# Kernel optimization log

Hardware: AMD Instinct MI355X
Metric: run time of the kernel (lower is better)

## Reference

```python
import jax, jax.numpy as jnp
import numpy as np

D_MODEL = 2048
D_INNER = 4096
D_XB = 1024
D_STATE = 64
HEADDIM = 64
NHEADS = D_INNER // HEADDIM      # 64
NXB = D_XB // HEADDIM
D_CONV = 4
CHUNK = 128
EPS = 1e-5
D_FF = 8192
CONV_DIM = D_XB + D_XB + D_INNER             # conv over [x, B, C]
D_IN_PROJ = D_INNER + D_XB + D_XB + D_INNER + NHEADS  # z, x, B, C, dt


def setup_inputs() -> dict:
    key = jax.random.key(0)
    ks = jax.random.split(key, 8)
    s = 0.02
    return {
        "hidden_states": jax.random.normal(ks[0], (2, 2048, D_MODEL), jnp.float32),
        "in_proj_w": jax.random.normal(ks[1], (D_MODEL, D_IN_PROJ), jnp.float32) * s,
        "conv_w": jax.random.normal(ks[2], (CONV_DIM, D_CONV), jnp.float32) * 0.1,
        "conv_b": jnp.zeros((CONV_DIM,), jnp.float32),
        "dt_bias": jnp.log(jnp.expm1(jnp.linspace(0.001, 0.1, NHEADS, dtype=jnp.float32))),
        "A_log": jnp.log(jnp.linspace(1.0, 16.0, NHEADS, dtype=jnp.float32)),
        "D": jnp.ones((NHEADS,), jnp.float32),
        "norm_w": jnp.ones((D_INNER,), jnp.float32),
        "out_proj_w": jax.random.normal(ks[3], (D_INNER, D_MODEL), jnp.float32) * s,
        "ln1_w": jnp.ones((D_MODEL,), jnp.float32),
        "ln2_w": jnp.ones((D_MODEL,), jnp.float32),
        "gate_w": jax.random.normal(ks[4], (D_MODEL, D_FF), jnp.float32) * s,
        "up_w": jax.random.normal(ks[5], (D_MODEL, D_FF), jnp.float32) * s,
        "down_w": jax.random.normal(ks[6], (D_FF, D_MODEL), jnp.float32) * s,
    }


def rmsnorm(x, w, eps=EPS):
    return x * jax.lax.rsqrt(jnp.mean(x * x, axis=-1, keepdims=True) + eps) * w


def causal_depthwise_conv(x, w, b):
    # x: [b, l, c], w: [c, k] depthwise causal conv
    k = w.shape[1]
    xp = jnp.pad(x, ((0, 0), (k - 1, 0), (0, 0)))
    out = jax.lax.conv_general_dilated(
        xp.transpose(0, 2, 1), w[:, None, :], (1,), "VALID",
        feature_group_count=x.shape[-1])
    return out.transpose(0, 2, 1) + b


def ssd_chunked(xdt, dA, Bm, Cm):
    # Mamba2 SSD chunked scan. xdt: [b,l,h,p] (x*dt), dA: [b,l,h] (dt*A), Bm/Cm: [b,l,h,n]
    b, l, h, p = xdt.shape
    n = Bm.shape[-1]
    c, q = l // CHUNK, CHUNK
    xdt = xdt.reshape(b, c, q, h, p)
    Bm = Bm.reshape(b, c, q, h, n)
    Cm = Cm.reshape(b, c, q, h, n)
    dA = dA.reshape(b, c, q, h).transpose(0, 3, 1, 2)   # [b,h,c,q]
    dAc = jnp.cumsum(dA, axis=-1)                        # [b,h,c,q]
    # intra-chunk (diagonal blocks)
    seg = dAc[..., :, None] - dAc[..., None, :]          # [b,h,c,q,q]
    mask = jnp.tril(jnp.ones((q, q), bool))
    Lm = jnp.where(mask, jnp.exp(seg), 0.0)
    Y_diag = jnp.einsum("bcqhn,bcshn,bhcqs,bcshp->bcqhp", Cm, Bm, Lm, xdt)
    # per-chunk final states
    decay_states = jnp.exp(dAc[..., -1:] - dAc)          # [b,h,c,q]
    states = jnp.einsum("bcqhn,bhcq,bcqhp->bchpn", Bm, decay_states, xdt)
    chunk_decay = jnp.exp(dAc[..., -1])                  # [b,h,c]
    def step(carry, inp):
        s, d = inp
        new = s + d[:, :, None, None] * carry
        return new, carry
    init = jnp.zeros((b, h, p, n), xdt.dtype)
    _, prevs = jax.lax.scan(step, init,
                            (states.transpose(1, 0, 2, 3, 4),
                             chunk_decay.transpose(2, 0, 1)))
    # prevs: [c,b,h,p,n] = state entering each chunk; inter-chunk contribution
    Y_off = jnp.einsum("bcqhn,cbhpn,bhcq->bcqhp", Cm, prevs, jnp.exp(dAc))
    return (Y_diag + Y_off).reshape(b, l, h, p)


def mamba2(x, in_proj_w, conv_w, conv_b, dt_bias, A_log, Dp, norm_w, out_proj_w):
    b, l, _ = x.shape
    zxbcdt = x @ in_proj_w
    z, xb, Bc, Cc, dt = jnp.split(
        zxbcdt, [D_INNER, D_INNER + D_XB, D_INNER + 2 * D_XB, 2 * D_INNER + 2 * D_XB], axis=-1)
    xBC = jax.nn.silu(causal_depthwise_conv(jnp.concatenate([xb, Bc, Cc], -1), conv_w, conv_b))
    xb, Bc, Cc = jnp.split(xBC, [D_XB, 2 * D_XB], axis=-1)
    dt = jax.nn.softplus(dt + dt_bias)                   # [b,l,h]
    A = -jnp.exp(A_log)                                  # [h]
    rep = NHEADS // NXB
    x_h = jnp.repeat(xb.reshape(b, l, NXB, HEADDIM), rep, axis=2)   # [b,l,h,p]
    B_h = jnp.repeat(Bc.reshape(b, l, NXB, D_STATE), rep, axis=2)   # [b,l,h,n]
    C_h = Cc.reshape(b, l, NHEADS, D_STATE)
    y = ssd_chunked(x_h * dt[..., None], dt * A, B_h, C_h)
    y = y + Dp[None, None, :, None] * x_h
    y = y.reshape(b, l, D_INNER)
    y = rmsnorm(y * jax.nn.silu(z), norm_w)
    return y @ out_proj_w


def reference(hidden_states, in_proj_w, conv_w, conv_b, dt_bias, A_log, D,
              norm_w, out_proj_w, ln1_w, ln2_w, gate_w, up_w, down_w):
    residual = hidden_states
    h = rmsnorm(hidden_states, ln1_w)
    h = residual + mamba2(h, in_proj_w, conv_w, conv_b, dt_bias, A_log, D, norm_w, out_proj_w)
    residual = h
    h2 = rmsnorm(h, ln2_w)
    mlp = (jax.nn.silu(h2 @ gate_w) * (h2 @ up_w)) @ down_w
    return residual + mlp
```

## Files before the change

kernel.cpp:

```cpp
#include <hip/hip_runtime.h>
#include <hip/hip_bf16.h>
#include <stdint.h>

#define TOK     4096
#define LSEQ    2048
#define DMODEL  2048
#define DINNER  4096
#define DXB     1024
#define DIP     10304
#define NPROJ   10240
#define CONVDIM 6144
#define DFF     8192
#define NH      64
#define CHUNK   128
#define NCHUNK  16
#define EPSF    1e-5f

typedef __hip_bfloat16 bf16_t;
typedef __bf16 bf16x8 __attribute__((ext_vector_type(8)));
typedef float f32x4 __attribute__((ext_vector_type(4)));

__device__ __forceinline__ float siluf(float x) { return x / (1.f + __expf(-x)); }
__device__ __forceinline__ float bf2f(bf16_t h) { return __bfloat162float(h); }
__device__ __forceinline__ float bits2f(unsigned short u) { return __uint_as_float((unsigned)u << 16); }
__device__ __forceinline__ unsigned short f2bits(float f) {
  union { bf16_t h; unsigned short u; } cv; cv.h = __float2bfloat16(f); return cv.u;
}
__device__ __forceinline__ void gload_lds16(const void* g, void* l) {
  __builtin_amdgcn_global_load_lds((const __attribute__((address_space(1))) void*)g,
                                   (__attribute__((address_space(3))) void*)l, 16, 0, 0);
}

__global__ void k_tcvt(const float* __restrict__ in, bf16_t* __restrict__ out,
                       int R, int C, int rs, int r_off, int c_off) {
  __shared__ float tile[32][33];
  int c0 = blockIdx.x * 32, r0 = blockIdx.y * 32;
  int tx = threadIdx.x, ty = threadIdx.y;
  for (int i = 0; i < 32; i += 8)
    tile[ty + i][tx] = in[(size_t)(r_off + r0 + ty + i) * rs + c_off + c0 + tx];
  __syncthreads();
  for (int i = 0; i < 32; i += 8)
    out[(size_t)(c0 + ty + i) * R + r0 + tx] = __float2bfloat16(tile[tx][ty + i]);
}

__global__ __launch_bounds__(256) void k_rmsnorm_bf16(const float* __restrict__ x,
                                                      const float* __restrict__ w,
                                                      bf16_t* __restrict__ out, int D) {
  int row = blockIdx.x, tid = threadIdx.x;
  const float* xr = x + (size_t)row * D;
  float ss = 0.f;
  for (int j = tid; j < D; j += 256) { float v = xr[j]; ss += v * v; }
  __shared__ float sbuf[4];
  for (int o = 32; o > 0; o >>= 1) ss += __shfl_down(ss, o, 64);
  if ((tid & 63) == 0) sbuf[tid >> 6] = ss;
  __syncthreads();
  float rinv = rsqrtf((sbuf[0] + sbuf[1] + sbuf[2] + sbuf[3]) / D + EPSF);
  bf16_t* orow = out + (size_t)row * D;
  for (int j = tid; j < D; j += 256) orow[j] = __float2bfloat16(xr[j] * rinv * w[j]);
}

__global__ __launch_bounds__(256) void k_gemm(const bf16_t* __restrict__ A,
                                              const bf16_t* __restrict__ Bt,
                                              const float* auxf,
                                              void* outp, void* out2,
                                              int M, int N, int K, int mode) {
  __shared__ unsigned short As[128][32];
  __shared__ unsigned short Bs[128][32];
  const int tid = threadIdx.x;
  const int n0 = blockIdx.x * 128, m0 = blockIdx.y * 128;
  const int lane = tid & 63, w = tid >> 6;
  const int wm = (w >> 1) * 64, wn = (w & 1) * 64;
  const int l16 = lane & 15, quad = lane >> 4;

  const int srow = lane >> 2;
  const int scol = (lane & 3) * 8;
  const unsigned short* Ag = (const unsigned short*)A + (size_t)(m0 + w * 32 + srow) * K + scol;
  const unsigned short* Bg = (const unsigned short*)Bt + (size_t)(n0 + w * 32 + srow) * K + scol;
  const size_t K16 = (size_t)16 * K;
  unsigned short* lA0 = &As[w * 32][0];
  unsigned short* lA1 = &As[w * 32 + 16][0];
  unsigned short* lB0 = &Bs[w * 32][0];
  unsigned short* lB1 = &Bs[w * 32 + 16][0];

  f32x4 acc[4][4] = {};
  for (int k0 = 0; k0 < K; k0 += 32) {
    __syncthreads();
    gload_lds16(Ag, lA0); gload_lds16(Ag + K16, lA1);
    gload_lds16(Bg, lB0); gload_lds16(Bg + K16, lB1);
    Ag += 32; Bg += 32;
    __syncthreads();
    bf16x8 af[4], bfv[4];
#pragma unroll
    for (int mi = 0; mi < 4; mi++) af[mi] = *(const bf16x8*)&As[wm + mi * 16 + l16][quad * 8];
#pragma unroll
    for (int ni = 0; ni < 4; ni++) bfv[ni] = *(const bf16x8*)&Bs[wn + ni * 16 + l16][quad * 8];
#pragma unroll
    for (int mi = 0; mi < 4; mi++)
#pragma unroll
      for (int ni = 0; ni < 4; ni++)
        acc[mi][ni] = __builtin_amdgcn_mfma_f32_16x16x32_bf16(af[mi], bfv[ni], acc[mi][ni], 0, 0, 0);
  }
#pragma unroll
  for (int mi = 0; mi < 4; mi++) {
    const int gm = m0 + wm + mi * 16 + quad * 4;
#pragma unroll
    for (int ni = 0; ni < 4; ni++) {
      const int gn = n0 + wn + ni * 16 + l16;
#pragma unroll
      for (int r = 0; r < 4; r++) {
        const size_t idx = (size_t)(gm + r) * N + gn;
        float v = acc[mi][ni][r];
        if (mode == 0) {
          ((float*)outp)[idx] = v + (auxf ? auxf[idx] : 0.f);
        } else if (mode == 1) {
          ((bf16_t*)outp)[idx] = __float2bfloat16(siluf(v));
        } else if (mode == 2) {
          bf16_t* o = (bf16_t*)outp;
          o[idx] = __float2bfloat16(v * bf2f(o[idx]));
        } else {
          if (gn < DINNER)
            ((bf16_t*)outp)[(size_t)(gm + r) * DINNER + gn] = __float2bfloat16(v);
          else
            ((bf16_t*)out2)[(size_t)(gm + r) * CONVDIM + (gn - DINNER)] = __float2bfloat16(v);
        }
      }
    }
  }
}

__global__ __launch_bounds__(256) void k_conv(const bf16_t* __restrict__ xr,
                                              const float* __restrict__ cw,
                                              const float* __restrict__ cb,
                                              bf16_t* __restrict__ xBC) {
  const int row = blockIdx.x;
  const int t = row & (LSEQ - 1);
  const float4* wv = (const float4*)cw;
  const float4* bv = (const float4*)cb;
  for (int c4 = threadIdx.x; c4 < CONVDIM / 4; c4 += 256) {
    const int c = c4 * 4;
    float4 w0 = wv[c], w1 = wv[c + 1], w2 = wv[c + 2], w3 = wv[c + 3];
    float4 bb = bv[c4];
    const bf16_t* base = xr + (size_t)row * CONVDIM + c;
    ushort4 u0 = *(const ushort4*)base;
    ushort4 u1 = {0,0,0,0}, u2 = {0,0,0,0}, u3 = {0,0,0,0};
    if (t >= 1) u1 = *(const ushort4*)(base - CONVDIM);
    if (t >= 2) u2 = *(const ushort4*)(base - 2 * CONVDIM);
    if (t >= 3) u3 = *(const ushort4*)(base - 3 * CONVDIM);
    ushort4 o;
    o.x = f2bits(siluf(bb.x + w0.x*bits2f(u3.x) + w0.y*bits2f(u2.x) + w0.z*bits2f(u1.x) + w0.w*bits2f(u0.x)));
    o.y = f2bits(siluf(bb.y + w1.x*bits2f(u3.y) + w1.y*bits2f(u2.y) + w1.z*bits2f(u1.y) + w1.w*bits2f(u0.y)));
    o.z = f2bits(siluf(bb.z + w2.x*bits2f(u3.z) + w2.y*bits2f(u2.z) + w2.z*bits2f(u1.z) + w2.w*bits2f(u0.z)));
    o.w = f2bits(siluf(bb.w + w3.x*bits2f(u3.w) + w3.y*bits2f(u2.w) + w3.z*bits2f(u1.w) + w3.w*bits2f(u0.w)));
    *(ushort4*)&xBC[(size_t)row * CONVDIM + c] = o;
  }
}

__global__ __launch_bounds__(256) void k_dt(const float* __restrict__ hs,
                                            const float* __restrict__ ln1,
                                            const float* __restrict__ Wip,
                                            const float* __restrict__ dt_bias,
                                            float* __restrict__ dt) {
  const int row = blockIdx.x, tid = threadIdx.x;
  __shared__ float xs[DMODEL];
  __shared__ float red[4][64];
  __shared__ float sbuf[4];
  const float* xr = hs + (size_t)row * DMODEL;
  float ss = 0.f;
  for (int j = tid; j < DMODEL; j += 256) { float v = xr[j]; ss += v * v; }
  for (int o = 32; o > 0; o >>= 1) ss += __shfl_down(ss, o, 64);
  if ((tid & 63) == 0) sbuf[tid >> 6] = ss;
  __syncthreads();
  float rinv = rsqrtf((sbuf[0] + sbuf[1] + sbuf[2] + sbuf[3]) / DMODEL + EPSF);
  for (int j = tid; j < DMODEL; j += 256) xs[j] = xr[j] * rinv * ln1[j];
  __syncthreads();
  const int h = tid & 63, kq = tid >> 6;
  float acc = 0.f;
  for (int k = kq * 512; k < (kq + 1) * 512; k++)
    acc += xs[k] * Wip[(size_t)k * DIP + 2 * DINNER + 2 * DXB + h];
  red[kq][h] = acc;
  __syncthreads();
  if (tid < 64) {
    float v = red[0][tid] + red[1][tid] + red[2][tid] + red[3][tid] + dt_bias[tid];
    float sp = (v > 20.f) ? v : log1pf(__expf(v));
    dt[(size_t)row * NH + tid] = sp;
  }
}

__global__ void k_dacum(const float* __restrict__ dt, const float* __restrict__ A_log,
                        float* __restrict__ dAc, float* __restrict__ cdec) {
  const int bh = blockIdx.x;
  const int b = bh >> 6, h = bh & 63;
  const int q = threadIdx.x;
  const float Ah = -__expf(A_log[h]);
  __shared__ float s[CHUNK];
  for (int c = 0; c < NCHUNK; c++) {
    int row = b * LSEQ + c * CHUNK + q;
    float v = dt[(size_t)row * NH + h] * Ah;
    s[q] = v;
    __syncthreads();
    for (int off = 1; off < CHUNK; off <<= 1) {
      float tadd = (q >= off) ? s[q - off] : 0.f;
      __syncthreads();
      s[q] += tadd;
      __syncthreads();
    }
    float r = s[q];
    dAc[((size_t)bh * NCHUNK + c) * CHUNK + q] = r;
    if (q == CHUNK - 1) cdec[bh * NCHUNK + c] = __expf(r);
    __syncthreads();
  }
}

__global__ __launch_bounds__(256) void k_states(const bf16_t* __restrict__ xBC,
                                                const float* __restrict__ dtp,
                                                const float* __restrict__ dAc,
                                                float* __restrict__ states) {
  const int blk = blockIdx.x;
  const int h = blk & 63, c = (blk >> 6) & 15, b = blk >> 10;
  const int tid = threadIdx.x;
  const int n0 = (tid >> 4) * 4, p0 = (tid & 15) * 4;
  const int rowb = b * LSEQ + c * CHUNK;
  const int boff = DXB + (h >> 2) * 64, xoff = (h >> 2) * 64;
  __shared__ float Bq[64][64];
  __shared__ float xq[64][64];
  __shared__ float dac_s[CHUNK];
  if (tid < CHUNK) dac_s[tid] = dAc[((size_t)(b * 64 + h) * NCHUNK + c) * CHUNK + tid];
  __syncthreads();
  const float last = dac_s[CHUNK - 1];
  f32x4 acc[4] = {};
  for (int half = 0; half < 2; half++) {
    __syncthreads();
    for (int idx = tid; idx < 64 * 64; idx += 256) {
      int q = idx >> 6, col = idx & 63;
      int row = rowb + half * 64 + q;
      float dec = __expf(last - dac_s[half * 64 + q]);
      const bf16_t* src = xBC + (size_t)row * CONVDIM;
      Bq[q][col] = bf2f(src[boff + col]) * dec;
      xq[q][col] = bf2f(src[xoff + col]) * dtp[(size_t)row * NH + h];
    }
    __syncthreads();
    for (int q = 0; q < 64; q++) {
      f32x4 bv = *(const f32x4*)&Bq[q][n0];
      f32x4 xv = *(const f32x4*)&xq[q][p0];
#pragma unroll
      for (int r = 0; r < 4; r++) acc[r] += bv[r] * xv;
    }
  }
  float* sb = states + (size_t)blk * 4096;
#pragma unroll
  for (int r = 0; r < 4; r++) *(f32x4*)&sb[(n0 + r) * 64 + p0] = acc[r];
}

__global__ __launch_bounds__(256) void k_scan(const float* __restrict__ states,
                                              const float* __restrict__ cdec,
                                              float* __restrict__ prevs) {
  const int gid = blockIdx.x * 256 + threadIdx.x;
  const int e = gid & 4095;
  const int h = (gid >> 12) & 63;
  const int b = gid >> 18;
  float carry = 0.f;
  for (int c = 0; c < NCHUNK; c++) {
    size_t idx = ((size_t)((b * 16 + c) * 64 + h)) * 4096 + e;
    prevs[idx] = carry;
    carry = states[idx] + cdec[(b * 64 + h) * NCHUNK + c] * carry;
  }
}

__global__ __launch_bounds__(256) void k_yout(const bf16_t* __restrict__ xBC,
                                              const float* __restrict__ dtp,
                                              const float* __restrict__ dAc,
                                              const float* __restrict__ prevs,
                                              const float* __restrict__ Dp,
                                              bf16_t* __restrict__ y) {
  const int blk = blockIdx.x;
  const int h = blk & 63, c = (blk >> 6) & 15, b = blk >> 10;
  const int tid = threadIdx.x;
  const int io = (tid >> 4) * 8, p0 = (tid & 15) * 4;
  const int si = (tid & 15), sj = (tid >> 4) * 2;
  const int rowb = b * LSEQ + c * CHUNK;
  const int xoff = (h >> 2) * 64, boff = DXB + (h >> 2) * 64, coff = 2 * DXB + h * 64;

  __shared__ float Call[128 * 65];
  __shared__ float BX[32 * 68];
  __shared__ __align__(16) char smS[32 * 132 * 4];
  __shared__ float dac_s[CHUNK];
  __shared__ float dt_s[CHUNK];
  float* Stile = (float*)smS;
  float* pv = (float*)smS;

  if (tid < CHUNK) {
    dac_s[tid] = dAc[((size_t)(b * 64 + h) * NCHUNK + c) * CHUNK + tid];
    dt_s[tid] = dtp[(size_t)(rowb + tid) * NH + h];
  }
  for (int idx = tid; idx < 128 * 64; idx += 256) {
    int i = idx >> 6, n = idx & 63;
    Call[i * 65 + n] = bf2f(xBC[(size_t)(rowb + i) * CONVDIM + coff + n]);
  }
  __syncthreads();

  const float Dh = Dp[h];
  f32x4 acc[8] = {};

  for (int jb = 0; jb < 4; jb++) {
    if (jb) __syncthreads();
    for (int idx = tid; idx < 32 * 64; idx += 256) {
      int q = idx >> 6, n = idx & 63;
      BX[q * 68 + n] = bf2f(xBC[(size_t)(rowb + jb * 32 + q) * CONVDIM + boff + n]);
    }
    __syncthreads();
    {
      float accS0[8] = {}, accS1[8] = {};
      const float* brow0 = &BX[sj * 68];
      const float* brow1 = &BX[(sj + 1) * 68];
      for (int n = 0; n < 64; n++) {
        float b0 = brow0[n], b1 = brow1[n];
#pragma unroll
        for (int r = 0; r < 8; r++) {
          float cv = Call[(si + 16 * r) * 65 + n];
          accS0[r] += b0 * cv;
          accS1[r] += b1 * cv;
        }
      }
      const int jg0 = jb * 32 + sj;
      const float dj0 = dac_s[jg0], dj1 = dac_s[jg0 + 1];
#pragma unroll
      for (int r = 0; r < 8; r++) {
        int i = si + 16 * r;
        float di = dac_s[i];
        Stile[sj * 132 + i]       = (jg0 <= i)     ? __expf(di - dj0) * accS0[r] : 0.f;
        Stile[(sj + 1) * 132 + i] = (jg0 + 1 <= i) ? __expf(di - dj1) * accS1[r] : 0.f;
      }
    }
    __syncthreads();
    for (int idx = tid; idx < 32 * 64; idx += 256) {
      int q = idx >> 6, p = idx & 63;
      BX[q * 68 + p] = bf2f(xBC[(size_t)(rowb + jb * 32 + q) * CONVDIM + xoff + p]) * dt_s[jb * 32 + q];
    }
    __syncthreads();
    for (int j = 0; j < 32; j++) {
      f32x4 s0 = *(const f32x4*)&Stile[j * 132 + io];
      f32x4 s1 = *(const f32x4*)&Stile[j * 132 + io + 4];
      f32x4 xv = *(const f32x4*)&BX[j * 68 + p0];
#pragma unroll
      for (int r = 0; r < 4; r++) acc[r] += s0[r] * xv;
#pragma unroll
      for (int r = 0; r < 4; r++) acc[4 + r] += s1[r] * xv;
    }
    if ((io >> 5) == jb) {
#pragma unroll
      for (int r = 0; r < 8; r++) {
        int i = io + r;
        float f = Dh / dt_s[i];
        f32x4 xv = *(const f32x4*)&BX[(i - jb * 32) * 68 + p0];
        acc[r] += f * xv;
      }
    }
  }
  __syncthreads();
  for (int idx = tid; idx < 128 * 64; idx += 256) {
    int i = idx >> 6, n = idx & 63;
    Call[i * 65 + n] *= __expf(dac_s[i]);
  }
  {
    const float* pvsrc = prevs + (size_t)blk * 4096;
    for (int idx = tid; idx < 64 * 64; idx += 256) pv[idx] = pvsrc[idx];
  }
  __syncthreads();
  for (int n = 0; n < 64; n++) {
    f32x4 pvv = *(const f32x4*)&pv[n * 64 + p0];
#pragma unroll
    for (int r = 0; r < 8; r++) acc[r] += Call[(io + r) * 65 + n] * pvv;
  }
#pragma unroll
  for (int r = 0; r < 8; r++) {
    int row = rowb + io + r;
    ushort4 st;
    st.x = f2bits(acc[r][0]); st.y = f2bits(acc[r][1]);
    st.z = f2bits(acc[r][2]); st.w = f2bits(acc[r][3]);
    *(ushort4*)&y[(size_t)row * DINNER + h * 64 + p0] = st;
  }
}

__global__ __launch_bounds__(256) void k_gatenorm(const bf16_t* __restrict__ y,
                                                  const bf16_t* __restrict__ z,
                                                  const float* __restrict__ nw,
                                                  bf16_t* __restrict__ outp) {
  const int row = blockIdx.x, tid = threadIdx.x;
  const bf16_t* yr = y + (size_t)row * DINNER;
  const bf16_t* zr = z + (size_t)row * DINNER;
  float vals[16];
  float ss = 0.f;
#pragma unroll
  for (int k = 0; k < 16; k++) {
    int j = tid + k * 256;
    float v = bf2f(yr[j]) * siluf(bf2f(zr[j]));
    vals[k] = v; ss += v * v;
  }
  __shared__ float sbuf[4];
  for (int o = 32; o > 0; o >>= 1) ss += __shfl_down(ss, o, 64);
  if ((tid & 63) == 0) sbuf[tid >> 6] = ss;
  __syncthreads();
  float rinv = rsqrtf((sbuf[0] + sbuf[1] + sbuf[2] + sbuf[3]) / DINNER + EPSF);
  bf16_t* orow = outp + (size_t)row * DINNER;
#pragma unroll
  for (int k = 0; k < 16; k++) {
    int j = tid + k * 256;
    orow[j] = __float2bfloat16(vals[k] * rinv * nw[j]);
  }
}

__global__ void k_diag(float* out, float mb) { out[0] = mb; }

static constexpr size_t OFF_WBUF = 0;
static constexpr size_t SZ_WBUF  = (size_t)NPROJ * DMODEL * 2;
static constexpr size_t OFF_Z    = OFF_WBUF + SZ_WBUF;
static constexpr size_t SZ_Z     = (size_t)TOK * DINNER * 2;
static constexpr size_t OFF_XBC  = OFF_Z + SZ_Z;
static constexpr size_t SZ_XBC   = (size_t)TOK * CONVDIM * 2;
static constexpr size_t OFF_DT   = OFF_XBC + SZ_XBC;
static constexpr size_t SZ_DT    = (size_t)TOK * NH * 4;
static constexpr size_t OFF_DAC  = OFF_DT + SZ_DT;
static constexpr size_t SZ_DAC   = (size_t)TOK * NH * 4;
static constexpr size_t OFF_CDEC = OFF_DAC + SZ_DAC;
static constexpr size_t SZ_CDEC  = (size_t)2 * 64 * NCHUNK * 4;
static constexpr size_t OFF_G    = OFF_CDEC + ((SZ_CDEC + 4095) & ~(size_t)4095);
static constexpr size_t SZ_G     = (size_t)2 * NCHUNK * 64 * 4096 * 4;
static constexpr size_t OFF_H    = OFF_G + SZ_G;
static constexpr size_t SZ_H     = (size_t)TOK * CONVDIM * 2;
static constexpr size_t OFF_I    = OFF_H + SZ_H;
static constexpr size_t SZ_I     = (size_t)2 * NCHUNK * 64 * 4096 * 4;
static constexpr size_t WS_NEED  = OFF_I + SZ_I;

extern "C" void kernel_launch(void* const* d_in, const int* in_sizes, int n_in,
                              void* d_out, int out_size, void* d_ws, size_t ws_size,
                              hipStream_t stream) {
  (void)in_sizes; (void)n_in; (void)out_size;
  if (ws_size < WS_NEED) {
    k_diag<<<1, 1, 0, stream>>>((float*)d_out, (float)(ws_size / 1048576.0));
    return;
  }

  const float* hidden     = (const float*)d_in[0];
  const float* in_proj_w  = (const float*)d_in[1];
  const float* conv_w     = (const float*)d_in[2];
  const float* conv_b     = (const float*)d_in[3];
  const float* dt_bias    = (const float*)d_in[4];
  const float* A_log      = (const float*)d_in[5];
  const float* Dv         = (const float*)d_in[6];
  const float* norm_w     = (const float*)d_in[7];
  const float* out_proj_w = (const float*)d_in[8];
  const float* ln1_w      = (const float*)d_in[9];
  const float* ln2_w      = (const float*)d_in[10];
  const float* gate_w     = (const float*)d_in[11];
  const float* up_w       = (const float*)d_in[12];
  const float* down_w     = (const float*)d_in[13];

  char* ws = (char*)d_ws;
  bf16_t* Wbuf  = (bf16_t*)(ws + OFF_WBUF);
  bf16_t* z     = (bf16_t*)(ws + OFF_Z);
  bf16_t* xBC   = (bf16_t*)(ws + OFF_XBC);
  float*  hbuf  = (float*)(ws + OFF_XBC);
  float*  dtb   = (float*)(ws + OFF_DT);
  float*  dAc   = (float*)(ws + OFF_DAC);
  float*  cdec  = (float*)(ws + OFF_CDEC);
  float*  prevs = (float*)(ws + OFF_G);
  bf16_t* h2n   = (bf16_t*)(ws + OFF_G);
  bf16_t* xbcr  = (bf16_t*)(ws + OFF_H);
  bf16_t* yn    = (bf16_t*)(ws + OFF_H);
  bf16_t* act   = (bf16_t*)(ws + OFF_H);
  bf16_t* xn1   = (bf16_t*)(ws + OFF_I);
  float*  states= (float*)(ws + OFF_I);
  bf16_t* y     = (bf16_t*)(ws + OFF_I);

  dim3 tb(32, 8);

  k_tcvt<<<dim3(NPROJ / 32, DMODEL / 32), tb, 0, stream>>>(in_proj_w, Wbuf, DMODEL, NPROJ, DIP, 0, 0);
  k_rmsnorm_bf16<<<TOK, 256, 0, stream>>>(hidden, ln1_w, xn1, DMODEL);
  k_gemm<<<dim3(NPROJ / 128, TOK / 128), 256, 0, stream>>>(xn1, Wbuf, nullptr, z, xbcr, TOK, NPROJ, DMODEL, 3);
  k_conv<<<TOK, 256, 0, stream>>>(xbcr, conv_w, conv_b, xBC);
  k_dt<<<TOK, 256, 0, stream>>>(hidden, ln1_w, in_proj_w, dt_bias, dtb);
  k_dacum<<<128, 128, 0, stream>>>(dtb, A_log, dAc, cdec);
  k_states<<<2048, 256, 0, stream>>>(xBC, dtb, dAc, states);
  k_scan<<<2048, 256, 0, stream>>>(states, cdec, prevs);
  k_yout<<<2048, 256, 0, stream>>>(xBC, dtb, dAc, prevs, Dv, y);
  k_gatenorm<<<TOK, 256, 0, stream>>>(y, z, norm_w, yn);
  k_tcvt<<<dim3(DMODEL / 32, DINNER / 32), tb, 0, stream>>>(out_proj_w, Wbuf, DINNER, DMODEL, DMODEL, 0, 0);
  k_gemm<<<dim3(DMODEL / 128, TOK / 128), 256, 0, stream>>>(yn, Wbuf, hidden, hbuf, nullptr, TOK, DMODEL, DINNER, 0);

  k_rmsnorm_bf16<<<TOK, 256, 0, stream>>>(hbuf, ln2_w, h2n, DMODEL);
  for (int g = 0; g < 2; g++) {
    const int HF = DFF / 2;
    k_tcvt<<<dim3(HF / 32, DMODEL / 32), tb, 0, stream>>>(gate_w, Wbuf, DMODEL, HF, DFF, 0, g * HF);
    k_gemm<<<dim3(HF / 128, TOK / 128), 256, 0, stream>>>(h2n, Wbuf, nullptr, act, nullptr, TOK, HF, DMODEL, 1);
    k_tcvt<<<dim3(HF / 32, DMODEL / 32), tb, 0, stream>>>(up_w, Wbuf, DMODEL, HF, DFF, 0, g * HF);
    k_gemm<<<dim3(HF / 128, TOK / 128), 256, 0, stream>>>(h2n, Wbuf, nullptr, act, nullptr, TOK, HF, DMODEL, 2);
    k_tcvt<<<dim3(DMODEL / 32, HF / 32), tb, 0, stream>>>(down_w, Wbuf, HF, DMODEL, DMODEL, g * HF, 0);
    k_gemm<<<dim3(DMODEL / 128, TOK / 128), 256, 0, stream>>>(act, Wbuf, g == 0 ? hbuf : (float*)d_out,
                                                              d_out, nullptr, TOK, DMODEL, HF, 0);
  }
}
```

Measured before the change: 2.014 ms.

## Rewrite SSD chunk output kernel with bf16 MFMA for intra-chunk and state terms

Replaces the scalar fp32 FMA loops in k_yout with bf16 MFMA 16x16x32 matrix ops. The C·B^T score matrix, the decayed-C times previous-state product, and the masked-score times x·dt product all run on the matrix cores, with data staged in LDS as bf16 (transposed where needed). The goal is to cut ALU time in this per-chunk kernel. In exchange, intermediate scores and the states are rounded to bf16, which adds precision error, and the wave-level tiling skips upper-triangular blocks.

```diff
diff --git a/kernel.cpp b/kernel.cpp
--- a/kernel.cpp
+++ b/kernel.cpp
@@ -18,6 +18,7 @@
 
 typedef __hip_bfloat16 bf16_t;
 typedef __bf16 bf16x8 __attribute__((ext_vector_type(8)));
+typedef unsigned short u16x8 __attribute__((ext_vector_type(8)));
 typedef float f32x4 __attribute__((ext_vector_type(4)));
 
 __device__ __forceinline__ float siluf(float x) { return x / (1.f + __expf(-x)); }
@@ -275,109 +276,142 @@
   const int blk = blockIdx.x;
   const int h = blk & 63, c = (blk >> 6) & 15, b = blk >> 10;
   const int tid = threadIdx.x;
-  const int io = (tid >> 4) * 8, p0 = (tid & 15) * 4;
-  const int si = (tid & 15), sj = (tid >> 4) * 2;
+  const int lane = tid & 63, w = tid >> 6;
+  const int l16 = lane & 15, quad = lane >> 4;
   const int rowb = b * LSEQ + c * CHUNK;
   const int xoff = (h >> 2) * 64, boff = DXB + (h >> 2) * 64, coff = 2 * DXB + h * 64;
 
-  __shared__ float Call[128 * 65];
-  __shared__ float BX[32 * 68];
-  __shared__ __align__(16) char smS[32 * 132 * 4];
+  __shared__ __align__(16) unsigned short CtX[128 * 72];
+  __shared__ __align__(16) unsigned short BtP[128 * 136];
+  __shared__ __align__(16) unsigned short pvT[64 * 72];
   __shared__ float dac_s[CHUNK];
   __shared__ float dt_s[CHUNK];
-  float* Stile = (float*)smS;
-  float* pv = (float*)smS;
 
   if (tid < CHUNK) {
     dac_s[tid] = dAc[((size_t)(b * 64 + h) * NCHUNK + c) * CHUNK + tid];
     dt_s[tid] = dtp[(size_t)(rowb + tid) * NH + h];
   }
-  for (int idx = tid; idx < 128 * 64; idx += 256) {
-    int i = idx >> 6, n = idx & 63;
-    Call[i * 65 + n] = bf2f(xBC[(size_t)(rowb + i) * CONVDIM + coff + n]);
-  }
-  __syncthreads();
-
-  const float Dh = Dp[h];
-  f32x4 acc[8] = {};
-
-  for (int jb = 0; jb < 4; jb++) {
-    if (jb) __syncthreads();
-    for (int idx = tid; idx < 32 * 64; idx += 256) {
-      int q = idx >> 6, n = idx & 63;
-      BX[q * 68 + n] = bf2f(xBC[(size_t)(rowb + jb * 32 + q) * CONVDIM + boff + n]);
-    }
-    __syncthreads();
-    {
-      float accS0[8] = {}, accS1[8] = {};
-      const float* brow0 = &BX[sj * 68];
-      const float* brow1 = &BX[(sj + 1) * 68];
-      for (int n = 0; n < 64; n++) {
-        float b0 = brow0[n], b1 = brow1[n];
-#pragma unroll
-        for (int r = 0; r < 8; r++) {
-          float cv = Call[(si + 16 * r) * 65 + n];
-          accS0[r] += b0 * cv;
-          accS1[r] += b1 * cv;
-        }
-      }
-      const int jg0 = jb * 32 + sj;
-      const float dj0 = dac_s[jg0], dj1 = dac_s[jg0 + 1];
-#pragma unroll
-      for (int r = 0; r < 8; r++) {
-        int i = si + 16 * r;
-        float di = dac_s[i];
-        Stile[sj * 132 + i]       = (jg0 <= i)     ? __expf(di - dj0) * accS0[r] : 0.f;
-        Stile[(sj + 1) * 132 + i] = (jg0 + 1 <= i) ? __expf(di - dj1) * accS1[r] : 0.f;
-      }
-    }
-    __syncthreads();
-    for (int idx = tid; idx < 32 * 64; idx += 256) {
-      int q = idx >> 6, p = idx & 63;
-      BX[q * 68 + p] = bf2f(xBC[(size_t)(rowb + jb * 32 + q) * CONVDIM + xoff + p]) * dt_s[jb * 32 + q];
-    }
-    __syncthreads();
-    for (int j = 0; j < 32; j++) {
-      f32x4 s0 = *(const f32x4*)&Stile[j * 132 + io];
-      f32x4 s1 = *(const f32x4*)&Stile[j * 132 + io + 4];
-      f32x4 xv = *(const f32x4*)&BX[j * 68 + p0];
-#pragma unroll
-      for (int r = 0; r < 4; r++) acc[r] += s0[r] * xv;
-#pragma unroll
-      for (int r = 0; r < 4; r++) acc[4 + r] += s1[r] * xv;
-    }
-    if ((io >> 5) == jb) {
-#pragma unroll
-      for (int r = 0; r < 8; r++) {
-        int i = io + r;
-        float f = Dh / dt_s[i];
-        f32x4 xv = *(const f32x4*)&BX[(i - jb * 32) * 68 + p0];
-        acc[r] += f * xv;
-      }
-    }
-  }
-  __syncthreads();
-  for (int idx = tid; idx < 128 * 64; idx += 256) {
-    int i = idx >> 6, n = idx & 63;
-    Call[i * 65 + n] *= __expf(dac_s[i]);
+  for (int idx = tid; idx < 1024; idx += 256) {
+    const int i = idx >> 3, e0 = (idx & 7) * 8;
+    const unsigned short* src = (const unsigned short*)xBC + (size_t)(rowb + i) * CONVDIM;
+    *(u16x8*)&CtX[i * 72 + e0] = *(const u16x8*)&src[coff + e0];
+    *(u16x8*)&BtP[i * 136 + e0] = *(const u16x8*)&src[boff + e0];
   }
   {
     const float* pvsrc = prevs + (size_t)blk * 4096;
-    for (int idx = tid; idx < 64 * 64; idx += 256) pv[idx] = pvsrc[idx];
-  }
-  __syncthreads();
-  for (int n = 0; n < 64; n++) {
-    f32x4 pvv = *(const f32x4*)&pv[n * 64 + p0];
-#pragma unroll
-    for (int r = 0; r < 8; r++) acc[r] += Call[(io + r) * 65 + n] * pvv;
-  }
-#pragma unroll
-  for (int r = 0; r < 8; r++) {
-    int row = rowb + io + r;
-    ushort4 st;
-    st.x = f2bits(acc[r][0]); st.y = f2bits(acc[r][1]);
-    st.z = f2bits(acc[r][2]); st.w = f2bits(acc[r][3]);
-    *(ushort4*)&y[(size_t)row * DINNER + h * 64 + p0] = st;
+    for (int idx = tid; idx < 1024; idx += 256) {
+      const int n = idx >> 4, p0 = (idx & 15) * 4;
+      f32x4 v = *(const f32x4*)&pvsrc[n * 64 + p0];
+#pragma unroll
+      for (int r = 0; r < 4; r++) pvT[(p0 + r) * 72 + n] = f2bits(v[r]);
+    }
+  }
+  __syncthreads();
+
+  const int wm = (w >> 1) * 64, wn = (w & 1) * 64;
+  f32x4 acc1[4][4] = {};
+  if (wm >= wn) {
+#pragma unroll
+    for (int kk = 0; kk < 2; kk++) {
+      bf16x8 af[4], bv[4];
+#pragma unroll
+      for (int mi = 0; mi < 4; mi++)
+        af[mi] = *(const bf16x8*)&CtX[(wm + mi * 16 + l16) * 72 + kk * 32 + quad * 8];
+#pragma unroll
+      for (int ni = 0; ni < 4; ni++)
+        bv[ni] = *(const bf16x8*)&BtP[(wn + ni * 16 + l16) * 136 + kk * 32 + quad * 8];
+#pragma unroll
+      for (int mi = 0; mi < 4; mi++)
+#pragma unroll
+        for (int ni = 0; ni < 4; ni++)
+          acc1[mi][ni] = __builtin_amdgcn_mfma_f32_16x16x32_bf16(af[mi], bv[ni], acc1[mi][ni], 0, 0, 0);
+    }
+  }
+  __syncthreads();
+
+#pragma unroll
+  for (int mi = 0; mi < 4; mi++) {
+#pragma unroll
+    for (int r = 0; r < 4; r++) {
+      const int i = wm + mi * 16 + quad * 4 + r;
+      const float di = dac_s[i];
+#pragma unroll
+      for (int ni = 0; ni < 4; ni++) {
+        const int j = wn + ni * 16 + l16;
+        const float v = (j <= i) ? __expf(di - dac_s[j]) * acc1[mi][ni][r] : 0.f;
+        BtP[i * 136 + j] = f2bits(v);
+      }
+    }
+  }
+  for (int idx = tid; idx < 1024; idx += 256) {
+    const int i = idx >> 3, e0 = (idx & 7) * 8;
+    const float sc = __expf(dac_s[i]);
+    u16x8 v = *(u16x8*)&CtX[i * 72 + e0];
+#pragma unroll
+    for (int r = 0; r < 8; r++) v[r] = f2bits(bits2f(v[r]) * sc);
+    *(u16x8*)&CtX[i * 72 + e0] = v;
+  }
+  __syncthreads();
+
+  const int wm2 = w * 32;
+  f32x4 acc2[2][4] = {};
+#pragma unroll
+  for (int kk = 0; kk < 2; kk++) {
+    bf16x8 af[2], bv[4];
+#pragma unroll
+    for (int mi = 0; mi < 2; mi++)
+      af[mi] = *(const bf16x8*)&CtX[(wm2 + mi * 16 + l16) * 72 + kk * 32 + quad * 8];
+#pragma unroll
+    for (int ni = 0; ni < 4; ni++)
+      bv[ni] = *(const bf16x8*)&pvT[(ni * 16 + l16) * 72 + kk * 32 + quad * 8];
+#pragma unroll
+    for (int mi = 0; mi < 2; mi++)
+#pragma unroll
+      for (int ni = 0; ni < 4; ni++)
+        acc2[mi][ni] = __builtin_amdgcn_mfma_f32_16x16x32_bf16(af[mi], bv[ni], acc2[mi][ni], 0, 0, 0);
+  }
+  __syncthreads();
+
+  for (int idx = tid; idx < 1024; idx += 256) {
+    const int j = idx >> 3, p0 = (idx & 7) * 8;
+    u16x8 v = *(const u16x8*)((const unsigned short*)xBC + (size_t)(rowb + j) * CONVDIM + xoff + p0);
+    const float dtj = dt_s[j];
+#pragma unroll
+    for (int r = 0; r < 8; r++) CtX[(p0 + r) * 136 + j] = f2bits(bits2f(v[r]) * dtj);
+  }
+  __syncthreads();
+
+#pragma unroll
+  for (int kk = 0; kk < 4; kk++) {
+    bf16x8 af[2], bv[4];
+#pragma unroll
+    for (int mi = 0; mi < 2; mi++)
+      af[mi] = *(const bf16x8*)&BtP[(wm2 + mi * 16 + l16) * 136 + kk * 32 + quad * 8];
+#pragma unroll
+    for (int ni = 0; ni < 4; ni++)
+      bv[ni] = *(const bf16x8*)&CtX[(ni * 16 + l16) * 136 + kk * 32 + quad * 8];
+#pragma unroll
+    for (int mi = 0; mi < 2; mi++)
+#pragma unroll
+      for (int ni = 0; ni < 4; ni++)
+        acc2[mi][ni] = __builtin_amdgcn_mfma_f32_16x16x32_bf16(af[mi], bv[ni], acc2[mi][ni], 0, 0, 0);
+  }
+
+  const float Dh = Dp[h];
+#pragma unroll
+  for (int mi = 0; mi < 2; mi++) {
+#pragma unroll
+    for (int r = 0; r < 4; r++) {
+      const int i = wm2 + mi * 16 + quad * 4 + r;
+      const float df = Dh / dt_s[i];
+      bf16_t* orow = y + (size_t)(rowb + i) * DINNER + h * 64;
+#pragma unroll
+      for (int ni = 0; ni < 4; ni++) {
+        const int p = ni * 16 + l16;
+        const float v = acc2[mi][ni][r] + df * bits2f(CtX[p * 136 + i]);
+        orow[p] = __float2bfloat16(v);
+      }
+    }
   }
 }
 
```

Result: faster. 1.807 ms (-10.2%).
